# Kernel optimization log

Measured on AMD Instinct MI355X. Metric: run time of the kernel, lower is better.

The kernel has to match this reference:

```python
import jax, jax.numpy as jnp
import numpy as np

B, C, L, M, EMB, HID = 32, 64, 8192, 32, 256, 64

def setup_inputs() -> dict:
    key = jax.random.key(0)
    ks = jax.random.split(key, 14)
    s_w = 1.0 / (C * C)
    s_a = 1.0 / EMB
    return {
        "x": jax.random.normal(ks[0], (B, C, L), jnp.float32),
        "emb": jax.random.normal(ks[1], (B, EMB), jnp.float32),
        "weights_pos": s_w * jax.random.normal(ks[2], (C, C, M, 2), jnp.float32),
        "weights_neg": s_w * jax.random.normal(ks[3], (C, C, M, 2), jnp.float32),
        "A_real_pos": s_a * jax.random.normal(ks[4], (M, EMB), jnp.float32),
        "A_imag_pos": s_a * jax.random.normal(ks[5], (M, EMB), jnp.float32),
        "A_real_neg": s_a * jax.random.normal(ks[6], (M, EMB), jnp.float32),
        "A_imag_neg": s_a * jax.random.normal(ks[7], (M, EMB), jnp.float32),
        "tm_w1": 0.05 * jax.random.normal(ks[8], (HID, EMB), jnp.float32),
        "tm_b1": jnp.zeros((HID,), jnp.float32),
        "tm_w2": 0.05 * jax.random.normal(ks[9], (2 * C, HID), jnp.float32),
        "tm_b2": jnp.zeros((2 * C,), jnp.float32),
        "lin_w": 0.05 * jax.random.normal(ks[10], (C, C), jnp.float32),
        "lin_b": jnp.zeros((C,), jnp.float32),
    }

def reference(x, emb, weights_pos, weights_neg, A_real_pos, A_imag_pos,
              A_real_neg, A_imag_neg, tm_w1, tm_b1, tm_w2, tm_b2, lin_w, lin_b):
    b, c, l = x.shape
    m = weights_pos.shape[2]
    k = l // 2 + 1
    # ---- SpectralConv1d branch ----
    x_ft = jnp.fft.rfft(x, norm="ortho")  # [B,C,K] complex
    wp = weights_pos[..., 0] + 1j * weights_pos[..., 1]  # [Ci,Co,M]
    wn = weights_neg[..., 0] + 1j * weights_neg[..., 1]
    phi_p = (emb @ A_real_pos.T) + 1j * (emb @ A_imag_pos.T)  # [B,M]
    phi_n = (emb @ A_real_neg.T) + 1j * (emb @ A_imag_neg.T)
    out_pos = jnp.einsum("bim,iom->bom", x_ft[:, :, :m], wp) * phi_p[:, None, :]
    out_neg = jnp.einsum("bim,iom->bom", x_ft[:, :, k - m:], wn) * phi_n[:, None, :]
    out_ft = jnp.zeros((b, c, k), dtype=x_ft.dtype)
    out_ft = out_ft.at[:, :, :m].set(out_pos).at[:, :, k - m:].set(out_neg)
    x1 = jnp.fft.irfft(out_ft, n=l, norm="ortho")  # [B,C,L]
    # ---- Conv1DTime branch (FiLM-style) ----
    h = jax.nn.silu(emb @ tm_w1.T + tm_b1)          # [B,HID]
    gb = h @ tm_w2.T + tm_b2                         # [B,2C]
    gamma, beta = gb[:, :c], gb[:, c:]
    xl = jnp.einsum("bcl,oc->bol", x, lin_w) + lin_b[None, :, None]
    x2 = xl * (1.0 + gamma[:, :, None]) + beta[:, :, None]
    return jax.nn.silu(x1 + x2)
```

## Files before the change

kernel.cpp:

```cpp
#include <hip/hip_runtime.h>
#include <math.h>

#define L_ 8192
#define EMB_ 256
#define HID_ 64

typedef __attribute__((ext_vector_type(8))) short bf16x8;
typedef __attribute__((ext_vector_type(4))) float f32x4;
typedef __attribute__((ext_vector_type(4))) int i32x4;

#define OFF_TFB  0
#define OFF_TLB  262144
#define OFF_AFB  524288
#define OFF_XFRP 917504
#define OFF_B2   3014656
#define OFF_PHI  3016704
#define OFF_GB   3020800
#define OFF_WT   3024896
#define OFF_XT   3549184

__device__ inline int pkbf(float a, float b) {
    int r;
    asm volatile("v_cvt_pk_bf16_f32 %0, %1, %2" : "=v"(r) : "v"(a), "v"(b));
    return r;
}
__device__ inline bf16x8 asbf(i32x4 v) { union { i32x4 i; bf16x8 h; } u; u.i = v; return u.h; }
#define MFMA(A,B,C) __builtin_amdgcn_mfma_f32_16x16x32_bf16((A),(B),(C),0,0,0)

__device__ inline ushort f2bf(float v) {
    unsigned b = __float_as_uint(v);
    return (ushort)((b + 0x7FFFu + ((b >> 16) & 1u)) >> 16);
}
__device__ inline float bf2f(ushort h) { return __uint_as_float(((unsigned)h) << 16); }
__device__ inline float hwsin(float rev) { float r; asm("v_sin_f32 %0, %1" : "=v"(r) : "v"(rev)); return r; }
__device__ inline float hwcos(float rev) { float r; asm("v_cos_f32 %0, %1" : "=v"(r) : "v"(rev)); return r; }
__device__ inline unsigned permb(unsigned hi, unsigned lo, unsigned sel) {
    unsigned r;
    asm("v_perm_b32 %0, %1, %2, %3" : "=v"(r) : "v"(hi), "v"(lo), "v"(sel));
    return r;
}

__global__ __launch_bounds__(256) void k_init(ushort* __restrict__ TLB, ushort* __restrict__ TFB,
        const float* __restrict__ emb,
        const float* __restrict__ Arp, const float* __restrict__ Aip,
        const float* __restrict__ Arn, const float* __restrict__ Ain, float* __restrict__ phi,
        const float* __restrict__ w1, const float* __restrict__ b1,
        const float* __restrict__ w2, const float* __restrict__ b2, float* __restrict__ gb,
        const float* __restrict__ wpos, const float* __restrict__ wneg, float* __restrict__ WT) {
    int bid = blockIdx.x;
    if (bid < 4096) {
        int idx = bid * 256 + threadIdx.x;
        int f, l; ushort* dst;
        if (idx < 524288) {
            int u = idx;
            int e = u & 7, lane = (u >> 3) & 63, ct = (u >> 9) & 3, kstep = u >> 11;
            l = kstep * 32 + ((lane >> 4) << 3) + e;
            f = ct * 16 + (lane & 15);
            dst = TLB + u;
        } else {
            int u = idx - 524288;
            int e = u & 7, lane = (u >> 3) & 63, ts = (u >> 9) & 1, lt = u >> 10;
            l = lt * 16 + (lane & 15);
            f = ts * 32 + ((lane >> 4) << 3) + e;
            dst = TFB + u;
        }
        int fr = f & 31; bool sinp = (f & 32) != 0;
        int r = (fr * l) & (L_ - 1);
        float rev = (float)r * (1.0f / (float)L_);
        float v = sinp ? hwsin(rev) : hwcos(rev);
        *dst = f2bf(v);
    } else if (bid < 4112) {
        int tid = (bid - 4096) * 256 + threadIdx.x;
        int b = tid >> 7;
        int mm = (tid >> 2) & 31;
        int cmp = tid & 3;
        const float* A = (cmp == 0) ? Arp : (cmp == 1) ? Aip : (cmp == 2) ? Arn : Ain;
        const float4* e4 = (const float4*)(emb + b * EMB_);
        const float4* a4 = (const float4*)(A + mm * EMB_);
        float acc = 0.f;
        for (int q = 0; q < EMB_ / 4; ++q) {
            float4 ev = e4[q], av = a4[q];
            acc += ev.x * av.x + ev.y * av.y + ev.z * av.z + ev.w * av.w;
        }
        phi[tid] = acc;
    } else if (bid < 4144) {
        __shared__ float h[HID_];
        int b = bid - 4112, t = threadIdx.x;
        if (t < HID_) {
            const float4* e4 = (const float4*)(emb + b * EMB_);
            const float4* w4 = (const float4*)(w1 + t * EMB_);
            float acc = b1[t];
            for (int q = 0; q < EMB_ / 4; ++q) {
                float4 ev = e4[q], wv = w4[q];
                acc += ev.x * wv.x + ev.y * wv.y + ev.z * wv.z + ev.w * wv.w;
            }
            h[t] = acc / (1.f + expf(-acc));
        }
        __syncthreads();
        if (t < 128) {
            float g = b2[t];
            const float4* h4 = (const float4*)h;
            const float4* w4 = (const float4*)(w2 + t * HID_);
            for (int q = 0; q < HID_ / 4; ++q) {
                float4 hv = h4[q], wv = w4[q];
                g += hv.x * wv.x + hv.y * wv.y + hv.z * wv.z + hv.w * wv.w;
            }
            if (t < 64) gb[(b * 64 + t) * 2 + 0] = 1.f + g;
            else        gb[(b * 64 + (t - 64)) * 2 + 1] = g;
        }
    } else {
        int t = bid - 4144;
        int side = t >> 6, i = t & 63;
        const float* W = side ? wneg : wpos;
        const float* src = W + (size_t)i * 4096;
        int tid = threadIdx.x;
        #pragma unroll
        for (int j = 0; j < 8; ++j) {
            int u = tid + 256 * j;
            int mm = u >> 6, o = u & 63;
            float2 v = *(const float2*)(src + o * 64 + mm * 2);
            *(float2*)(WT + ((size_t)(side * 32 + mm)) * 8192 + i * 128 + o * 2) = v;
        }
    }
}

__global__ __launch_bounds__(256, 4) void k_dft(const float* __restrict__ x,
        const ushort* __restrict__ TLB, float* __restrict__ xfrp, unsigned* __restrict__ XT2) {
    __shared__ float sP[2][16][132];
    __shared__ unsigned sX[4][16][68];
    int stripe = blockIdx.x >> 3;
    int lseg = blockIdx.x & 7;
    int w = threadIdx.x >> 6;
    int lane = threadIdx.x & 63;
    int r0 = stripe * 16;
    int kb0 = lseg * 1024 + w * 256;

    f32x4 acc[8];
    #pragma unroll
    for (int i = 0; i < 8; ++i) acc[i] = (f32x4){0.f, 0.f, 0.f, 0.f};

    const i32x4* tb = (const i32x4*)TLB;
    int tbase = (kb0 >> 5) * 256 + lane;
    const i32x4 SM = {(int)0x80000000, (int)0x80000000, (int)0x80000000, (int)0x80000000};

    int lrow2 = lane >> 5;
    int lcol = (lane & 31) * 4;
    int jw = (lane & 31) * 2;
    int frow = lane & 15;
    int fj = (lane >> 4) * 4;

    #pragma unroll
    for (int c = 0; c < 2; ++c) {
        int cbase = kb0 + c * 128;
        float4 f0 = *(const float4*)(x + (size_t)(r0 + 0  + lrow2) * L_ + cbase + lcol);
        float4 f1 = *(const float4*)(x + (size_t)(r0 + 2  + lrow2) * L_ + cbase + lcol);
        float4 f2 = *(const float4*)(x + (size_t)(r0 + 4  + lrow2) * L_ + cbase + lcol);
        float4 f3 = *(const float4*)(x + (size_t)(r0 + 6  + lrow2) * L_ + cbase + lcol);
        float4 f4 = *(const float4*)(x + (size_t)(r0 + 8  + lrow2) * L_ + cbase + lcol);
        float4 f5 = *(const float4*)(x + (size_t)(r0 + 10 + lrow2) * L_ + cbase + lcol);
        float4 f6 = *(const float4*)(x + (size_t)(r0 + 12 + lrow2) * L_ + cbase + lcol);
        float4 f7 = *(const float4*)(x + (size_t)(r0 + 14 + lrow2) * L_ + cbase + lcol);
        #define STG(i, fv)                                                   \
            {                                                                \
                unsigned d0 = (unsigned)pkbf(fv.x, fv.y);                    \
                unsigned d1 = (unsigned)pkbf(fv.z, fv.w);                    \
                sX[w][i * 2 + lrow2][jw]     = d0;                           \
                sX[w][i * 2 + lrow2][jw + 1] = d1;                           \
            }
        STG(0, f0) STG(1, f1) STG(2, f2) STG(3, f3)
        STG(4, f4) STG(5, f5) STG(6, f6) STG(7, f7)
        #undef STG
        #pragma unroll
        for (int ks = 0; ks < 4; ++ks) {
            i32x4 av = *(const i32x4*)&sX[w][frow][ks * 16 + fj];
            bf16x8 AH = asbf(av);
            int ti = tbase + (c * 4 + ks) * 256;
            i32x4 t0 = tb[ti], t1 = tb[ti + 64], t2 = tb[ti + 128], t3 = tb[ti + 192];
            acc[0] = MFMA(AH, asbf(t0), acc[0]); acc[4] = MFMA(AH, asbf(t0 ^ SM), acc[4]);
            acc[1] = MFMA(AH, asbf(t1), acc[1]); acc[5] = MFMA(AH, asbf(t1 ^ SM), acc[5]);
            acc[2] = MFMA(AH, asbf(t2), acc[2]); acc[6] = MFMA(AH, asbf(t2 ^ SM), acc[6]);
            acc[3] = MFMA(AH, asbf(t3), acc[3]); acc[7] = MFMA(AH, asbf(t3 ^ SM), acc[7]);
        }
        {
            unsigned* xtc = XT2 + ((size_t)stripe * 4096 + (cbase >> 1)) * 16;
            int ch4 = (lane & 3) * 4;
            #pragma unroll
            for (int q = 0; q < 4; ++q) {
                int j = q * 16 + (lane >> 2);
                uint4 v;
                v.x = sX[w][ch4 + 0][j];
                v.y = sX[w][ch4 + 1][j];
                v.z = sX[w][ch4 + 2][j];
                v.w = sX[w][ch4 + 3][j];
                *(uint4*)(xtc + (size_t)(q * 256 + lane * 4)) = v;
            }
        }
    }
    int crow = (lane >> 4) << 2;
    int ccol = lane & 15;
    if (w < 2) {
        #pragma unroll
        for (int ct = 0; ct < 8; ++ct)
            #pragma unroll
            for (int r = 0; r < 4; ++r)
                sP[w][crow + r][ct * 16 + ccol] = acc[ct][r];
    }
    __syncthreads();
    if (w >= 2) {
        #pragma unroll
        for (int ct = 0; ct < 8; ++ct)
            #pragma unroll
            for (int r = 0; r < 4; ++r)
                sP[w - 2][crow + r][ct * 16 + ccol] += acc[ct][r];
    }
    __syncthreads();
    #pragma unroll
    for (int i = 0; i < 8; ++i) {
        int e = threadIdx.x + 256 * i;
        int rr = e & 15, cc = e >> 4;
        float s = sP[0][rr][cc] + sP[1][rr][cc];
        xfrp[((size_t)(lseg * 128 + cc)) * 2048 + r0 + rr] = s;
    }
}

__global__ __launch_bounds__(256) void k_mix(const float* __restrict__ xfrt,
        const float* __restrict__ WT,
        const float* __restrict__ phi, const float* __restrict__ lw,
        const float* __restrict__ lb, const float* __restrict__ gb,
        ushort* __restrict__ afb, float* __restrict__ bias2) {
    int bi = blockIdx.x;
    int tid = threadIdx.x;
    if (bi >= 256) {
        int b = bi - 256;
        ushort* dst = afb + (size_t)b * 24576;
        #pragma unroll
        for (int j = 0; j < 16; ++j) {
            int u = tid + 256 * j;
            int e = u & 7, lane = (u >> 3) & 63, mt = (u >> 9) & 3, ks2 = u >> 11;
            int c = mt * 16 + (lane & 15);
            int kk = ((lane >> 4) << 3) + e;
            float v = lw[c * 64 + ks2 * 32 + kk] * gb[(b * 64 + c) * 2];
            ushort hi = f2bf(v);
            int base = (((4 + ks2) * 4 + mt) * 64 + lane) * 16;
            dst[base + e] = hi;
            dst[base + 8 + e] = f2bf(v - bf2f(hi));
        }
        if (tid < 64) {
            float g1 = gb[(b * 64 + tid) * 2], be = gb[(b * 64 + tid) * 2 + 1];
            bias2[b * 64 + tid] = lb[tid] * g1 + be;
        }
        return;
    }
    __shared__ float sW[64][64][2];
    __shared__ float sXr[8][64], sXi[8][64];
    int bh = bi & 3, side = (bi >> 2) & 1, mm = bi >> 3;
    int slot = side ? (31 - mm) : mm;
    int colR = side ? (64 + slot) : mm;
    int colI = side ? (96 + slot) : (32 + mm);

    {
        const float4* wt = (const float4*)(WT + ((size_t)(side * 32 + mm)) * 8192);
        float* sWlin = &sW[0][0][0];
        #pragma unroll
        for (int j = 0; j < 8; ++j) {
            int u = tid + 256 * j;
            *(float4*)&sWlin[u * 4] = wt[u];
        }
    }
    {
        const float2* pR = (const float2*)(xfrt + (size_t)colR * 2048 + bh * 512);
        const float2* pI = (const float2*)(xfrt + (size_t)colI * 2048 + bh * 512);
        float2 aR = {0, 0}, aI = {0, 0};
        #pragma unroll
        for (int s = 0; s < 8; ++s) {
            float2 vR = pR[(size_t)s * 131072 + tid];
            float2 vI = pI[(size_t)s * 131072 + tid];
            aR.x += vR.x; aR.y += vR.y;
            aI.x += vI.x; aI.y += vI.y;
        }
        if (!side) { aI.x = -aI.x; aI.y = -aI.y; }
        *(float2*)&sXr[tid >> 5][(tid & 31) * 2] = aR;
        *(float2*)&sXi[tid >> 5][(tid & 31) * 2] = aI;
    }
    __syncthreads();

    int o = tid & 63, bg = tid >> 6;
    const float invL = 1.f / (float)L_;
    float fac = (slot == 0) ? invL : 2.f * invL;
    int comp = side ? 2 : 0;
    int e = slot & 7, kgrp = slot >> 3;
    int mt = o >> 4, lane = kgrp * 16 + (o & 15);
    #pragma unroll
    for (int bl = 0; bl < 2; ++bl) {
        int b_local = bg * 2 + bl;
        int b = bh * 8 + b_local;
        float sre = 0.f, sim = 0.f;
        #pragma unroll 16
        for (int i = 0; i < 64; ++i) {
            float wr = sW[i][o][0], wi = sW[i][o][1];
            float xr = sXr[b_local][i], xi = sXi[b_local][i];
            sre += xr * wr - xi * wi;
            sim += xr * wi + xi * wr;
        }
        const float* ph = &phi[(b * 32 + mm) * 4 + (side ? 2 : 0)];
        float phr = ph[0], phim = ph[1];
        float Pre = sre * phr - sim * phim;
        float Pim = sre * phim + sim * phr;
        float a = fac * Pre;
        float bcoef = (slot == 0) ? 0.f : (side ? 2.f * invL * Pim : -2.f * invL * Pim);
        ushort* dst = afb + (size_t)b * 24576;
        ushort hiA = f2bf(a);
        int baseA = ((comp * 4 + mt) * 64 + lane) * 16;
        dst[baseA + e] = hiA;
        dst[baseA + 8 + e] = f2bf(a - bf2f(hiA));
        ushort hiB = f2bf(bcoef);
        int baseB = (((comp + 1) * 4 + mt) * 64 + lane) * 16;
        dst[baseB + e] = hiB;
        dst[baseB + 8 + e] = f2bf(bcoef - bf2f(hiB));
    }
}

#define TPART(ts)                                                                        \
    {                                                                                    \
        i32x4 bh_[2];                                                                    \
        _Pragma("unroll")                                                                \
        for (int nj = 0; nj < 2; ++nj)                                                   \
            bh_[nj] = tb[((lt0 + nj) * 2 + (ts)) * 64 + lane];                           \
        _Pragma("unroll")                                                                \
        for (int mt = 0; mt < 4; ++mt) {                                                 \
            i32x4 ah0 = ab[(((ts) * 4 + mt) * 64 + lane) * 2];                           \
            i32x4 ah1 = ab[(((2 + (ts)) * 4 + mt) * 64 + lane) * 2];                     \
            bf16x8 AH0 = asbf(ah0), AH1 = asbf(ah1);                                     \
            _Pragma("unroll")                                                            \
            for (int nj = 0; nj < 2; ++nj) {                                             \
                acc[mt][nj] = MFMA(AH0, asbf(bh_[nj]), acc[mt][nj]);                     \
                acc[mt][nj] = MFMA(AH1, asbf(bh_[nj] ^ SM), acc[mt][nj]);                \
            }                                                                            \
        }                                                                                \
    }

#define XPART(ts, xv0, xv1)                                                              \
    {                                                                                    \
        bf16x8 XH0 = asbf(xv0), XH1 = asbf(xv1);                                         \
        _Pragma("unroll")                                                                \
        for (int mt = 0; mt < 4; ++mt) {                                                 \
            i32x4 ah = ab[(((4 + (ts)) * 4 + mt) * 64 + lane) * 2];                      \
            bf16x8 AH = asbf(ah);                                                        \
            acc[mt][0] = MFMA(AH, XH0, acc[mt][0]);                                      \
            acc[mt][1] = MFMA(AH, XH1, acc[mt][1]);                                      \
        }                                                                                \
    }

#define XEXTRACT(q0, q1, dstvar)                                                         \
    dstvar = (i32x4){                                                                    \
        (int)permb((unsigned)q0[1], (unsigned)q0[0], sel),                               \
        (int)permb((unsigned)q0[3], (unsigned)q0[2], sel),                               \
        (int)permb((unsigned)q1[1], (unsigned)q1[0], sel),                               \
        (int)permb((unsigned)q1[3], (unsigned)q1[2], sel)};

__global__ __launch_bounds__(256, 3) void k_fuse(const unsigned* __restrict__ XT2,
        const ushort* __restrict__ TFB, const ushort* __restrict__ AFB,
        const float* __restrict__ bias2, float* __restrict__ out) {
    int b = blockIdx.x >> 6, lt = blockIdx.x & 63;
    int w = threadIdx.x >> 6, lane = threadIdx.x & 63;
    int col = lane & 15, kgrp = lane >> 4;
    int lbase = lt * 128 + w * 32;
    int lt0 = lbase >> 4;
    const i32x4* tb = (const i32x4*)TFB;
    const i32x4* ab = (const i32x4*)AFB + (size_t)b * 3072;
    const i32x4* xt4 = (const i32x4*)XT2;

    f32x4 acc[4][2];
    #pragma unroll
    for (int i = 0; i < 4; ++i)
        #pragma unroll
        for (int j = 0; j < 2; ++j) acc[i][j] = (f32x4){0.f, 0.f, 0.f, 0.f};

    int sm = (col & 1) ? (int)0x80008000 : 0;
    i32x4 SM = {sm, sm, sm, sm};
    unsigned sel = (col & 1) ? 0x07060302u : 0x05040100u;

    size_t i00 = ((size_t)(b * 4 + (kgrp >> 1)) * 4096 + ((lbase + col) >> 1)) * 4 + (kgrp & 1) * 2;
    size_t i01 = i00 + 8 * 4;
    size_t i10 = i00 + (size_t)2 * 4096 * 4;
    size_t i11 = i10 + 8 * 4;
    i32x4 q000 = xt4[i00], q001 = xt4[i00 + 1];
    i32x4 q010 = xt4[i01], q011 = xt4[i01 + 1];
    i32x4 q100 = xt4[i10], q101 = xt4[i10 + 1];
    i32x4 q110 = xt4[i11], q111 = xt4[i11 + 1];

    TPART(0)
    i32x4 xv00, xv01;
    XEXTRACT(q000, q001, xv00)
    XEXTRACT(q010, q011, xv01)
    XPART(0, xv00, xv01)
    TPART(1)
    i32x4 xv10, xv11;
    XEXTRACT(q100, q101, xv10)
    XEXTRACT(q110, q111, xv11)
    XPART(1, xv10, xv11)

    #pragma unroll
    for (int mt = 0; mt < 4; ++mt) {
        #pragma unroll
        for (int r = 0; r < 4; ++r) {
            int c = mt * 16 + kgrp * 4 + r;
            float bias = bias2[b * 64 + c];
            float* op = out + (size_t)(b * 64 + c) * L_ + lbase + col;
            #pragma unroll
            for (int nj = 0; nj < 2; ++nj) {
                float v = acc[mt][nj][r] + bias;
                op[nj * 16] = v / (1.f + __expf(-v));
            }
        }
    }
}

extern "C" void kernel_launch(void* const* d_in, const int* in_sizes, int n_in,
                              void* d_out, int out_size, void* d_ws, size_t ws_size,
                              hipStream_t stream) {
    const float* x    = (const float*)d_in[0];
    const float* emb  = (const float*)d_in[1];
    const float* wpos = (const float*)d_in[2];
    const float* wneg = (const float*)d_in[3];
    const float* Arp  = (const float*)d_in[4];
    const float* Aip  = (const float*)d_in[5];
    const float* Arn  = (const float*)d_in[6];
    const float* Ain  = (const float*)d_in[7];
    const float* w1   = (const float*)d_in[8];
    const float* b1   = (const float*)d_in[9];
    const float* w2   = (const float*)d_in[10];
    const float* b2   = (const float*)d_in[11];
    const float* lw   = (const float*)d_in[12];
    const float* lb   = (const float*)d_in[13];
    float* out = (float*)d_out;
    float* ws = (float*)d_ws;
    ushort*   TFB  = (ushort*)(ws + OFF_TFB);
    ushort*   TLB  = (ushort*)(ws + OFF_TLB);
    ushort*   AFB  = (ushort*)(ws + OFF_AFB);
    float*    XFRP = ws + OFF_XFRP;
    float*    B2   = ws + OFF_B2;
    float*    PHI  = ws + OFF_PHI;
    float*    GB   = ws + OFF_GB;
    float*    WT   = ws + OFF_WT;
    unsigned* XT2  = (unsigned*)(ws + OFF_XT);

    hipLaunchKernelGGL(k_init,  dim3(4272), dim3(256), 0, stream,
                       TLB, TFB, emb, Arp, Aip, Arn, Ain, PHI, w1, b1, w2, b2, GB,
                       wpos, wneg, WT);
    hipLaunchKernelGGL(k_dft,   dim3(1024), dim3(256), 0, stream, x, TLB, XFRP, XT2);
    hipLaunchKernelGGL(k_mix,   dim3(288),  dim3(256), 0, stream, XFRP, WT, PHI,
                       lw, lb, GB, AFB, B2);
    hipLaunchKernelGGL(k_fuse,  dim3(2048), dim3(256), 0, stream, XT2, TFB, AFB, B2, out);
}
```

Measured before the change: 66.18 us.

## Split DFT into single-wave blocks and move partial-sum reduction to mix kernel

```diff
diff --git a/kernel.cpp b/kernel.cpp
--- a/kernel.cpp
+++ b/kernel.cpp
@@ -13,11 +13,11 @@
 #define OFF_TLB  262144
 #define OFF_AFB  524288
 #define OFF_XFRP 917504
-#define OFF_B2   3014656
-#define OFF_PHI  3016704
-#define OFF_GB   3020800
-#define OFF_WT   3024896
-#define OFF_XT   3549184
+#define OFF_B2   9306112
+#define OFF_PHI  9308160
+#define OFF_GB   9312256
+#define OFF_WT   9316352
+#define OFF_XT   9840640
 
 __device__ inline int pkbf(float a, float b) {
     int r;
@@ -124,16 +124,15 @@
     }
 }
 
-__global__ __launch_bounds__(256, 4) void k_dft(const float* __restrict__ x,
+__global__ __launch_bounds__(64, 4) void k_dft(const float* __restrict__ x,
         const ushort* __restrict__ TLB, float* __restrict__ xfrp, unsigned* __restrict__ XT2) {
-    __shared__ float sP[2][16][132];
-    __shared__ unsigned sX[4][16][68];
-    int stripe = blockIdx.x >> 3;
-    int lseg = blockIdx.x & 7;
-    int w = threadIdx.x >> 6;
-    int lane = threadIdx.x & 63;
+    __shared__ float sBuf[16][132];
+    unsigned* sU = (unsigned*)&sBuf[0][0];
+    int stripe = blockIdx.x >> 5;
+    int lseg = blockIdx.x & 31;
+    int lane = threadIdx.x;
     int r0 = stripe * 16;
-    int kb0 = lseg * 1024 + w * 256;
+    int kb0 = lseg * 256;
 
     f32x4 acc[8];
     #pragma unroll
@@ -160,19 +159,21 @@
         float4 f5 = *(const float4*)(x + (size_t)(r0 + 10 + lrow2) * L_ + cbase + lcol);
         float4 f6 = *(const float4*)(x + (size_t)(r0 + 12 + lrow2) * L_ + cbase + lcol);
         float4 f7 = *(const float4*)(x + (size_t)(r0 + 14 + lrow2) * L_ + cbase + lcol);
+        __syncthreads();
         #define STG(i, fv)                                                   \
             {                                                                \
                 unsigned d0 = (unsigned)pkbf(fv.x, fv.y);                    \
                 unsigned d1 = (unsigned)pkbf(fv.z, fv.w);                    \
-                sX[w][i * 2 + lrow2][jw]     = d0;                           \
-                sX[w][i * 2 + lrow2][jw + 1] = d1;                           \
+                sU[(i * 2 + lrow2) * 68 + jw]     = d0;                      \
+                sU[(i * 2 + lrow2) * 68 + jw + 1] = d1;                      \
             }
         STG(0, f0) STG(1, f1) STG(2, f2) STG(3, f3)
         STG(4, f4) STG(5, f5) STG(6, f6) STG(7, f7)
         #undef STG
+        __syncthreads();
         #pragma unroll
         for (int ks = 0; ks < 4; ++ks) {
-            i32x4 av = *(const i32x4*)&sX[w][frow][ks * 16 + fj];
+            i32x4 av = *(const i32x4*)&sU[frow * 68 + ks * 16 + fj];
             bf16x8 AH = asbf(av);
             int ti = tbase + (c * 4 + ks) * 256;
             i32x4 t0 = tb[ti], t1 = tb[ti + 64], t2 = tb[ti + 128], t3 = tb[ti + 192];
@@ -188,38 +189,28 @@
             for (int q = 0; q < 4; ++q) {
                 int j = q * 16 + (lane >> 2);
                 uint4 v;
-                v.x = sX[w][ch4 + 0][j];
-                v.y = sX[w][ch4 + 1][j];
-                v.z = sX[w][ch4 + 2][j];
-                v.w = sX[w][ch4 + 3][j];
+                v.x = sU[(ch4 + 0) * 68 + j];
+                v.y = sU[(ch4 + 1) * 68 + j];
+                v.z = sU[(ch4 + 2) * 68 + j];
+                v.w = sU[(ch4 + 3) * 68 + j];
                 *(uint4*)(xtc + (size_t)(q * 256 + lane * 4)) = v;
             }
         }
     }
+    __syncthreads();
     int crow = (lane >> 4) << 2;
     int ccol = lane & 15;
-    if (w < 2) {
-        #pragma unroll
-        for (int ct = 0; ct < 8; ++ct)
-            #pragma unroll
-            for (int r = 0; r < 4; ++r)
-                sP[w][crow + r][ct * 16 + ccol] = acc[ct][r];
-    }
+    #pragma unroll
+    for (int ct = 0; ct < 8; ++ct)
+        #pragma unroll
+        for (int r = 0; r < 4; ++r)
+            sBuf[crow + r][ct * 16 + ccol] = acc[ct][r];
     __syncthreads();
-    if (w >= 2) {
-        #pragma unroll
-        for (int ct = 0; ct < 8; ++ct)
-            #pragma unroll
-            for (int r = 0; r < 4; ++r)
-                sP[w - 2][crow + r][ct * 16 + ccol] += acc[ct][r];
-    }
-    __syncthreads();
-    #pragma unroll
-    for (int i = 0; i < 8; ++i) {
-        int e = threadIdx.x + 256 * i;
+    #pragma unroll
+    for (int i = 0; i < 32; ++i) {
+        int e = lane + 64 * i;
         int rr = e & 15, cc = e >> 4;
-        float s = sP[0][rr][cc] + sP[1][rr][cc];
-        xfrp[((size_t)(lseg * 128 + cc)) * 2048 + r0 + rr] = s;
+        xfrp[((size_t)(lseg * 128 + cc)) * 2048 + r0 + rr] = sBuf[rr][cc];
     }
 }
 
@@ -272,7 +263,7 @@
         const float2* pI = (const float2*)(xfrt + (size_t)colI * 2048 + bh * 512);
         float2 aR = {0, 0}, aI = {0, 0};
         #pragma unroll
-        for (int s = 0; s < 8; ++s) {
+        for (int s = 0; s < 32; ++s) {
             float2 vR = pR[(size_t)s * 131072 + tid];
             float2 vI = pI[(size_t)s * 131072 + tid];
             aR.x += vR.x; aR.y += vR.y;
@@ -448,7 +439,7 @@
     hipLaunchKernelGGL(k_init,  dim3(4272), dim3(256), 0, stream,
                        TLB, TFB, emb, Arp, Aip, Arn, Ain, PHI, w1, b1, w2, b2, GB,
                        wpos, wneg, WT);
-    hipLaunchKernelGGL(k_dft,   dim3(1024), dim3(256), 0, stream, x, TLB, XFRP, XT2);
+    hipLaunchKernelGGL(k_dft,   dim3(4096), dim3(64),  0, stream, x, TLB, XFRP, XT2);
     hipLaunchKernelGGL(k_mix,   dim3(288),  dim3(256), 0, stream, XFRP, WT, PHI,
                        lw, lb, GB, AFB, B2);
     hipLaunchKernelGGL(k_fuse,  dim3(2048), dim3(256), 0, stream, XT2, TFB, AFB, B2, out);
```

Measured after the change: 71.83 us. 1.09x slower.
